# Kernel optimization log

Hardware: AMD Instinct MI355X
Metric: run time of the kernel (lower is better)

The kernel has to match this reference:

```python
import jax, jax.numpy as jnp
import numpy as np
import math

D_MODEL = 1024
NHEAD = 16
HEAD_DIM = D_MODEL // NHEAD
ROPE_BASE = 10000.0


def _rope(x):
    # x: [B, H, S, Dh]; rotate per the RoPE class (half-split variant)
    d = x.shape[-1]
    half = d // 2
    seq_len = x.shape[2]
    theta = 1.0 / (ROPE_BASE ** (jnp.arange(0, d, 2, dtype=jnp.float32) / d))  # [d/2]
    ang = jnp.arange(seq_len, dtype=jnp.float32)[:, None] * theta[None, :]      # [S, d/2]
    ang2 = jnp.concatenate([ang, ang], axis=-1)                                 # [S, d]
    cos_ = jnp.cos(ang2)[None, None, :, :]
    sin_ = jnp.sin(ang2)[None, None, :, :]
    neg_half = jnp.concatenate([-x[..., half:], x[..., :half]], axis=-1)
    return x * cos_ + neg_half * sin_


def setup_inputs() -> dict:
    key = jax.random.key(0)
    ks = jax.random.split(key, 10)
    B, S, D = 4, 2048, D_MODEL
    scale = 1.0 / math.sqrt(D)
    x = jax.random.normal(ks[0], (B, S, D), dtype=jnp.float32)
    Wq = jax.random.normal(ks[1], (D, D), dtype=jnp.float32) * scale
    bq = jnp.zeros((D,), dtype=jnp.float32)
    Wk = jax.random.normal(ks[2], (D, D), dtype=jnp.float32) * scale
    bk = jnp.zeros((D,), dtype=jnp.float32)
    Wv = jax.random.normal(ks[3], (D, D), dtype=jnp.float32) * scale
    bv = jnp.zeros((D,), dtype=jnp.float32)
    Wo = jax.random.normal(ks[4], (D, D), dtype=jnp.float32) * scale
    bo = jnp.zeros((D,), dtype=jnp.float32)
    # causal mask: mask==1 means masked (upper triangle)
    mask = jnp.triu(jnp.ones((S, S), dtype=jnp.int32), k=1)[None, None, :, :]
    return {"x": x, "Wq": Wq, "bq": bq, "Wk": Wk, "bk": bk,
            "Wv": Wv, "bv": bv, "Wo": Wo, "bo": bo, "mask": mask}


def reference(x, Wq, bq, Wk, bk, Wv, bv, Wo, bo, mask):
    B, S, D = x.shape
    H, Dh = NHEAD, HEAD_DIM

    def proj(W, b):
        y = jnp.einsum('bsd,ed->bse', x, W) + b  # torch Linear: x @ W.T + b
        return y.reshape(B, S, H, Dh).transpose(0, 2, 1, 3)  # [B,H,S,Dh]

    q = _rope(proj(Wq, bq))
    k = _rope(proj(Wk, bk))
    v = proj(Wv, bv)

    a = jnp.einsum('bhqd,bhkd->bhqk', q, k) / math.sqrt(Dh)  # [B,H,S,S]
    a = jnp.where(mask == 1, jnp.float32(-1e9), a)
    a = jax.nn.softmax(a, axis=-1)
    out = jnp.einsum('bhqk,bhkd->bhqd', a, v)                 # [B,H,S,Dh]
    out = out.transpose(0, 2, 1, 3).reshape(B, S, D)
    return jnp.einsum('bsd,ed->bse', out, Wo) + bo
```

## Files before the change

### kernel.cpp

```cpp
#include <hip/hip_runtime.h>
#include <stdint.h>

typedef unsigned short u16;
typedef __bf16 bf16x8 __attribute__((ext_vector_type(8)));
typedef __bf16 bf16x2 __attribute__((ext_vector_type(2)));
typedef float f32x4 __attribute__((ext_vector_type(4)));

#define SEQ    2048
#define NHEAD  16
#define DH     64
#define DMODEL 1024
#define NBH    64

__device__ __forceinline__ u16 cvt1(float f){
  union { __bf16 h; u16 u; } c; c.h = (__bf16)f; return c.u;
}
__device__ __forceinline__ uint32_t cvt2(float a, float b){
  union { bf16x2 v; uint32_t u; } c; c.v = bf16x2{(__bf16)a, (__bf16)b}; return c.u;
}
__device__ __forceinline__ int swz(int row){ return (((row&7)^((row>>3)&7))<<4); }

typedef const __attribute__((address_space(1))) uint32_t* gas_t;
typedef __attribute__((address_space(3))) uint32_t* las_t;
__device__ __forceinline__ void async16(const void* g, void* l){
  __builtin_amdgcn_global_load_lds((gas_t)g, (las_t)l, 16, 0, 0);
}

__global__ void prep(const float* __restrict__ x,  const float* __restrict__ Wq,
                     const float* __restrict__ Wk, const float* __restrict__ Wv,
                     const float* __restrict__ Wo,
                     u16* __restrict__ xb, u16* __restrict__ wqkv,
                     u16* __restrict__ wob, float* __restrict__ tab)
{
  const int bid = blockIdx.x, tid = threadIdx.x;
  if (bid < 6144){
    const float* src; u16* dst; int lb;
    if      (bid < 4096){ src = x;  dst = xb;              lb = bid; }
    else if (bid < 4608){ src = Wq; dst = wqkv;            lb = bid-4096; }
    else if (bid < 5120){ src = Wk; dst = wqkv + 1048576;  lb = bid-4608; }
    else if (bid < 5632){ src = Wv; dst = wqkv + 2097152;  lb = bid-5120; }
    else                { src = Wo; dst = wob;             lb = bid-5632; }
    const size_t off = (size_t)lb*2048 + tid*8;
    float4 a = *(const float4*)(src+off);
    float4 b = *(const float4*)(src+off+4);
    bf16x8 o = { (__bf16)a.x,(__bf16)a.y,(__bf16)a.z,(__bf16)a.w,
                 (__bf16)b.x,(__bf16)b.y,(__bf16)b.z,(__bf16)b.w };
    *(bf16x8*)(dst+off) = o;
  } else {
    const int t = (bid-6144)*256 + tid;
    const int s = t >> 5, j = t & 31;
    double freq = exp(-(double)(2*j)/64.0*log(10000.0));
    double ang = (double)s*freq;
    tab[s*64 + 2*j]     = (float)cos(ang);
    tab[s*64 + 2*j + 1] = (float)sin(ang);
  }
}

template<int MODE>
__global__ __launch_bounds__(256, 2)
void gemm_bt(const u16* __restrict__ A, const u16* __restrict__ W,
             const float* __restrict__ b0, const float* __restrict__ b1,
             const float* __restrict__ b2, float* __restrict__ fout,
             u16* __restrict__ dq, u16* __restrict__ dk, u16* __restrict__ dv,
             const float* __restrict__ tab)
{
  __shared__ u16 Ab[128*32];
  __shared__ u16 Bb[128*32];
  const int tid = threadIdx.x;
  const int lane = tid & 63;
  const int w = tid >> 6, wr = w >> 1, wc = w & 1;
  const int m0 = blockIdx.y * 128;
  const int n0 = blockIdx.x * 128;
  const int c0 = lane & 15, g = lane >> 4;

  f32x4 acc[4][4] = {};

  const int sr = tid >> 2;
  const int sc = (tid & 3) * 8;
  const u16* ga = A + (size_t)(m0 + sr) * DMODEL + sc;
  const u16* gb = W + (size_t)(n0 + sr) * DMODEL + sc;
  u16* la = Ab + sr*32 + sc;
  u16* lb = Bb + sr*32 + sc;

  for (int k0 = 0; k0 < DMODEL; k0 += 32) {
    __syncthreads();
    async16(ga + k0,             la);
    async16(ga + k0 + 64*DMODEL, la + 64*32);
    async16(gb + k0,             lb);
    async16(gb + k0 + 64*DMODEL, lb + 64*32);
    __syncthreads();
    bf16x8 afr[4], bfr[4];
#pragma unroll
    for (int i=0;i<4;i++) afr[i] = *(const bf16x8*)(Ab + (wr*64 + i*16 + c0)*32 + g*8);
#pragma unroll
    for (int j=0;j<4;j++) bfr[j] = *(const bf16x8*)(Bb + (wc*64 + j*16 + c0)*32 + g*8);
    __builtin_amdgcn_s_setprio(1);
#pragma unroll
    for (int i=0;i<4;i++)
#pragma unroll
      for (int j=0;j<4;j++)
        acc[i][j] = __builtin_amdgcn_mfma_f32_16x16x32_bf16(afr[i], bfr[j], acc[i][j], 0,0,0);
    __builtin_amdgcn_s_setprio(0);
  }

  const int nbase = n0 + wc*64;
  const int t = n0 >> 10;
  const float* bias = (MODE==1) ? b0 : (t==0) ? b0 : (t==1) ? b1 : b2;
  float bv4[4];
#pragma unroll
  for (int j=0;j<4;j++) bv4[j] = bias[(nbase & 1023) + j*16 + c0];

  if (MODE == 0) {
    u16* dst = (t==0) ? dq : (t==1) ? dk : dv;
    const float qs = (t==0) ? 0.18033688011f : 1.0f;
    const int h = (nbase >> 6) & (NHEAD-1);
#pragma unroll
    for (int i=0;i<4;i++){
      const int mbase = m0 + wr*64 + i*16 + g*4;
#pragma unroll
      for (int r=0;r<4;r++){
        const int mm = mbase + r;
        const int bb = mm >> 11, s = mm & (SEQ-1);
        const size_t rowbase = (((size_t)(bb*NHEAD + h))*SEQ + s)*DH;
        if (t < 2) {
#pragma unroll
          for (int j2=0;j2<2;j2++){
            const int dh = j2*16 + c0;
            const float xl = acc[i][j2][r]   + bv4[j2];
            const float xh = acc[i][j2+2][r] + bv4[j2+2];
            const float2 cs = *(const float2*)(tab + (size_t)s*64 + dh*2);
            dst[rowbase + dh]      = cvt1((xl*cs.x - xh*cs.y)*qs);
            dst[rowbase + dh + 32] = cvt1((xh*cs.x + xl*cs.y)*qs);
          }
        } else {
#pragma unroll
          for (int j=0;j<4;j++)
            dst[rowbase + j*16 + c0] = cvt1(acc[i][j][r] + bv4[j]);
        }
      }
    }
  } else {
#pragma unroll
    for (int i=0;i<4;i++){
      const int mbase = m0 + wr*64 + i*16 + g*4;
#pragma unroll
      for (int j=0;j<4;j++){
#pragma unroll
        for (int r=0;r<4;r++)
          fout[(size_t)(mbase + r) * DMODEL + nbase + j*16 + c0] = acc[i][j][r] + bv4[j];
      }
    }
  }
}

__global__ __launch_bounds__(256, 4)
void attn_fwd(const u16* __restrict__ Q, const u16* __restrict__ K,
              const u16* __restrict__ V, u16* __restrict__ O)
{
  __shared__ u16 Kb[2][64*64];
  __shared__ u16 Vt[2][64*64];
  const int bh = blockIdx.x;
  const int pair = blockIdx.y;
  const int tid = threadIdx.x, lane = tid & 63, w = tid >> 6;
  const int c0 = lane & 15, g = lane >> 4;
  const size_t hb = (size_t)bh * SEQ * DH;
  const int b = bh >> 4, h = bh & 15;

  const int boff  = tid*16;
  const int sw1   = boff  ^ swz(boff  >> 7);
  const int boff2 = boff + 4096;
  const int sw2   = boff2 ^ swz(boff2 >> 7);
  const int rp = tid >> 3, dc = tid & 7;
  const int kv0 = 2*rp;
  const int vpos = (kv0 & 0x23) | ((kv0 & 0x10) >> 2) | ((kv0 & 0x0C) << 1);
  union U4 { ushort4 v; u16 e[4]; };

#pragma unroll 1
  for (int half = 0; half < 2; half++){
    const int qt = half ? (31 - pair) : pair;
    const int qrow_base = qt*64 + w*16;
    const int jt_end = qt;
    const int q = qrow_base + c0;

    bf16x8 qf[2];
#pragma unroll
    for (int kc=0;kc<2;kc++)
      qf[kc] = *(const bf16x8*)(Q + hb + (size_t)q*DH + kc*32 + g*8);

    f32x4 oacc[4] = {};
    float mrun = -3.0e38f, lrun = 0.f;

    {
      const char* gk = (const char*)(K + hb);
      async16(gk + sw1, (char*)Kb[0] + boff);
      async16(gk + sw2, (char*)Kb[0] + boff2);
      const u16* gv = V + hb;
      U4 v0a, v0b, v1a, v1b;
      v0a.v = *(const ushort4*)(gv + (kv0  )*DH + dc*8);
      v0b.v = *(const ushort4*)(gv + (kv0  )*DH + dc*8 + 4);
      v1a.v = *(const ushort4*)(gv + (kv0+1)*DH + dc*8);
      v1b.v = *(const ushort4*)(gv + (kv0+1)*DH + dc*8 + 4);
#pragma unroll
      for (int e=0;e<8;e++){
        const int row = dc*8 + e;
        const int gbyte = row*128 + vpos*2;
        const u16 a   = (e<4) ? v0a.e[e] : v0b.e[e-4];
        const u16 bb2 = (e<4) ? v1a.e[e] : v1b.e[e-4];
        *(uint32_t*)((char*)Vt[0] + (gbyte ^ swz(row))) = (uint32_t)a | ((uint32_t)bb2 << 16);
      }
    }
    __syncthreads();

    U4 v0a, v0b, v1a, v1b;
    for (int jt = 0; jt <= jt_end; jt++){
      const int cur = jt & 1, nxt = cur ^ 1;
      const bool pre = (jt < jt_end);
      if (pre){
        const char* gk = (const char*)(K + hb + (size_t)(jt+1)*64*DH);
        async16(gk + sw1, (char*)Kb[nxt] + boff);
        async16(gk + sw2, (char*)Kb[nxt] + boff2);
        const u16* gv = V + hb + (size_t)(jt+1)*64*DH;
        v0a.v = *(const ushort4*)(gv + (kv0  )*DH + dc*8);
        v0b.v = *(const ushort4*)(gv + (kv0  )*DH + dc*8 + 4);
        v1a.v = *(const ushort4*)(gv + (kv0+1)*DH + dc*8);
        v1b.v = *(const ushort4*)(gv + (kv0+1)*DH + dc*8 + 4);
      }

      f32x4 sT[4] = {};
#pragma unroll
      for (int kc=0;kc<2;kc++){
        bf16x8 kf[4];
#pragma unroll
        for (int j=0;j<4;j++){
          const int rr = j*16 + c0;
          const int gb2 = rr*128 + kc*64 + g*16;
          kf[j] = *(const bf16x8*)((const char*)Kb[cur] + (gb2 ^ swz(rr)));
        }
        __builtin_amdgcn_s_setprio(1);
#pragma unroll
        for (int j=0;j<4;j++)
          sT[j] = __builtin_amdgcn_mfma_f32_16x16x32_bf16(kf[j], qf[kc], sT[j], 0,0,0);
        __builtin_amdgcn_s_setprio(0);
      }
      if (jt == jt_end){
#pragma unroll
        for (int j=0;j<4;j++)
#pragma unroll
          for (int r=0;r<4;r++){
            const int kv = jt*64 + j*16 + g*4 + r;
            sT[j][r] = (kv <= q) ? sT[j][r] : -3.0e38f;
          }
      }
      float mx = -3.0e38f;
#pragma unroll
      for (int j=0;j<4;j++)
#pragma unroll
        for (int r=0;r<4;r++) mx = fmaxf(mx, sT[j][r]);
      mx = fmaxf(mx, __shfl_xor(mx, 16));
      mx = fmaxf(mx, __shfl_xor(mx, 32));
      const bool grow = __any(mx > mrun + 8.0f);
      float corr = 1.0f;
      if (grow){
        const float mnew = fmaxf(mrun, mx);
        corr = exp2f(mrun - mnew);
        mrun = mnew;
      }
      bf16x8 pa0, pa1;
      float lsum = 0.f;
#pragma unroll
      for (int j=0;j<4;j++){
#pragma unroll
        for (int r=0;r<4;r++){
          const float p = exp2f(sT[j][r] - mrun);
          lsum += p;
          if (j<2) pa0[(j&1)*4 + r] = (__bf16)p;
          else     pa1[(j&1)*4 + r] = (__bf16)p;
        }
      }
      lsum += __shfl_xor(lsum, 16);
      lsum += __shfl_xor(lsum, 32);
      lrun = lrun*corr + lsum;
      if (grow){
#pragma unroll
        for (int d=0;d<4;d++)
#pragma unroll
          for (int r=0;r<4;r++) oacc[d][r] *= corr;
      }
#pragma unroll
      for (int kc=0;kc<2;kc++){
        const bf16x8 pa = kc ? pa1 : pa0;
        bf16x8 vf[4];
#pragma unroll
        for (int d=0; d<4; d++){
          const int rr = d*16 + c0;
          const int gb2 = rr*128 + kc*64 + g*16;
          vf[d] = *(const bf16x8*)((const char*)Vt[cur] + (gb2 ^ swz(rr)));
        }
        __builtin_amdgcn_s_setprio(1);
#pragma unroll
        for (int d=0; d<4; d++)
          oacc[d] = __builtin_amdgcn_mfma_f32_16x16x32_bf16(vf[d], pa, oacc[d], 0,0,0);
        __builtin_amdgcn_s_setprio(0);
      }

      if (pre){
#pragma unroll
        for (int e=0;e<8;e++){
          const int row = dc*8 + e;
          const int gbyte = row*128 + vpos*2;
          const u16 a   = (e<4) ? v0a.e[e] : v0b.e[e-4];
          const u16 bb2 = (e<4) ? v1a.e[e] : v1b.e[e-4];
          *(uint32_t*)((char*)Vt[nxt] + (gbyte ^ swz(row))) = (uint32_t)a | ((uint32_t)bb2 << 16);
        }
      }
      __syncthreads();
    }

    {
      const float inv = 1.0f / lrun;
      u16* orow = O + ((size_t)b*SEQ + q)*DMODEL + h*DH;
#pragma unroll
      for (int d=0;d<4;d++)
#pragma unroll
        for (int r2=0;r2<2;r2++)
          *(uint32_t*)(orow + d*16 + g*4 + 2*r2) =
            cvt2(oacc[d][2*r2]*inv, oacc[d][2*r2+1]*inv);
    }
  }
}

extern "C" void kernel_launch(void* const* d_in, const int* in_sizes, int n_in,
                              void* d_out, int out_size, void* d_ws, size_t ws_size,
                              hipStream_t stream)
{
  const float* x  = (const float*)d_in[0];
  const float* Wq = (const float*)d_in[1];
  const float* bq = (const float*)d_in[2];
  const float* Wk = (const float*)d_in[3];
  const float* bk = (const float*)d_in[4];
  const float* Wv = (const float*)d_in[5];
  const float* bv = (const float*)d_in[6];
  const float* Wo = (const float*)d_in[7];
  const float* bo = (const float*)d_in[8];

  const size_t MB = 1024*1024;
  char* ws = (char*)d_ws;
  u16*  xb   = (u16*)(ws);
  u16*  aw   = (u16*)(ws);
  u16*  vw   = (u16*)(ws + 16*MB);
  u16*  wqkv = (u16*)(ws + 32*MB);
  u16*  wob  = (u16*)(ws + 38*MB);
  float* tab = (float*)(ws + 41*MB);
  u16*  qw = (u16*)d_out;
  u16*  kw = (u16*)d_out + 8*MB;

  prep<<<dim3(6400), dim3(256), 0, stream>>>(x, Wq, Wk, Wv, Wo, xb, wqkv, wob, tab);

  gemm_bt<0><<<dim3(24, 64), dim3(256), 0, stream>>>(xb, wqkv, bq, bk, bv,
                                                     nullptr, qw, kw, vw, tab);

  attn_fwd<<<dim3(64, 16), dim3(256), 0, stream>>>(qw, kw, vw, aw);

  gemm_bt<1><<<dim3(8, 64), dim3(256), 0, stream>>>(aw, wob, bo, nullptr, nullptr,
                                                    (float*)d_out, nullptr, nullptr, nullptr, nullptr);
}
```

Measured before the change: 200.9 us.

## Use 256-row query tiles with 8 waves and 32x32 MFMA in attention

The attention kernel now processes 256-query tiles per block with 512 threads (8 waves of 32 rows each) instead of 64-query tiles with 4 waves. It uses 32x32x16 bf16 MFMAs, so each K/V tile staged in shared memory is reused by more queries and global K/V traffic drops. Waves whose rows are fully masked for a KV tile skip its compute but still join the barriers. The trade-offs are fewer blocks (256 instead of 1024), launch bounds allowing only one block per CU, coarser causal load balance, and idle waves on diagonal tiles.

Result: no change. 197.6 us (-1.7%).

```diff
diff --git a/kernel.cpp b/kernel.cpp
--- a/kernel.cpp
+++ b/kernel.cpp
@@ -5,6 +5,7 @@
 typedef __bf16 bf16x8 __attribute__((ext_vector_type(8)));
 typedef __bf16 bf16x2 __attribute__((ext_vector_type(2)));
 typedef float f32x4 __attribute__((ext_vector_type(4)));
+typedef float f32x16 __attribute__((ext_vector_type(16)));
 
 #define SEQ    2048
 #define NHEAD  16
@@ -153,7 +154,7 @@
   }
 }
 
-__global__ __launch_bounds__(256, 4)
+__global__ __launch_bounds__(512, 1)
 void attn_fwd(const u16* __restrict__ Q, const u16* __restrict__ K,
               const u16* __restrict__ V, u16* __restrict__ O)
 {
@@ -162,155 +163,136 @@
   const int bh = blockIdx.x;
   const int pair = blockIdx.y;
   const int tid = threadIdx.x, lane = tid & 63, w = tid >> 6;
-  const int c0 = lane & 15, g = lane >> 4;
+  const int c31 = lane & 31, hi = lane >> 5;
   const size_t hb = (size_t)bh * SEQ * DH;
   const int b = bh >> 4, h = bh & 15;
 
-  const int boff  = tid*16;
-  const int sw1   = boff  ^ swz(boff  >> 7);
-  const int boff2 = boff + 4096;
-  const int sw2   = boff2 ^ swz(boff2 >> 7);
-  const int rp = tid >> 3, dc = tid & 7;
+  const int boff = tid*16;
+  const int ksw  = boff ^ swz(boff >> 7);
+  const int rp = tid >> 4, dc = tid & 15;
   const int kv0 = 2*rp;
-  const int vpos = (kv0 & 0x23) | ((kv0 & 0x10) >> 2) | ((kv0 & 0x0C) << 1);
+  const int vpos = (kv0 & 0x33) | ((kv0 & 4) << 1) | ((kv0 & 8) >> 1);
   union U4 { ushort4 v; u16 e[4]; };
 
 #pragma unroll 1
   for (int half = 0; half < 2; half++){
-    const int qt = half ? (31 - pair) : pair;
-    const int qrow_base = qt*64 + w*16;
-    const int jt_end = qt;
-    const int q = qrow_base + c0;
-
-    bf16x8 qf[2];
-#pragma unroll
-    for (int kc=0;kc<2;kc++)
-      qf[kc] = *(const bf16x8*)(Q + hb + (size_t)q*DH + kc*32 + g*8);
-
-    f32x4 oacc[4] = {};
+    const int qt = half ? (7 - pair) : pair;
+    const int qrow_base = qt*256 + w*32;
+    const int jt_last  = 4*qt + 3;
+    const int jt_end_w = 4*qt + (w>>1);
+    const int q = qrow_base + c31;
+
+    bf16x8 qf[4];
+#pragma unroll
+    for (int kc=0;kc<4;kc++)
+      qf[kc] = *(const bf16x8*)(Q + hb + (size_t)q*DH + kc*16 + hi*8);
+
+    f32x16 oacc0 = {}, oacc1 = {};
     float mrun = -3.0e38f, lrun = 0.f;
 
     {
       const char* gk = (const char*)(K + hb);
-      async16(gk + sw1, (char*)Kb[0] + boff);
-      async16(gk + sw2, (char*)Kb[0] + boff2);
+      async16(gk + ksw, (char*)Kb[0] + boff);
       const u16* gv = V + hb;
-      U4 v0a, v0b, v1a, v1b;
-      v0a.v = *(const ushort4*)(gv + (kv0  )*DH + dc*8);
-      v0b.v = *(const ushort4*)(gv + (kv0  )*DH + dc*8 + 4);
-      v1a.v = *(const ushort4*)(gv + (kv0+1)*DH + dc*8);
-      v1b.v = *(const ushort4*)(gv + (kv0+1)*DH + dc*8 + 4);
-#pragma unroll
-      for (int e=0;e<8;e++){
-        const int row = dc*8 + e;
-        const int gbyte = row*128 + vpos*2;
-        const u16 a   = (e<4) ? v0a.e[e] : v0b.e[e-4];
-        const u16 bb2 = (e<4) ? v1a.e[e] : v1b.e[e-4];
-        *(uint32_t*)((char*)Vt[0] + (gbyte ^ swz(row))) = (uint32_t)a | ((uint32_t)bb2 << 16);
+      U4 va, vb;
+      va.v = *(const ushort4*)(gv + kv0*DH + dc*4);
+      vb.v = *(const ushort4*)(gv + (kv0+1)*DH + dc*4);
+#pragma unroll
+      for (int d=0; d<4; d++){
+        const int row = dc*4 + d;
+        *(uint32_t*)((char*)Vt[0] + ((row*128 + vpos*2) ^ swz(row))) =
+          (uint32_t)va.e[d] | ((uint32_t)vb.e[d] << 16);
       }
     }
     __syncthreads();
 
-    U4 v0a, v0b, v1a, v1b;
-    for (int jt = 0; jt <= jt_end; jt++){
+    U4 va, vb;
+    for (int jt = 0; jt <= jt_last; jt++){
       const int cur = jt & 1, nxt = cur ^ 1;
-      const bool pre = (jt < jt_end);
+      const bool pre = (jt < jt_last);
       if (pre){
         const char* gk = (const char*)(K + hb + (size_t)(jt+1)*64*DH);
-        async16(gk + sw1, (char*)Kb[nxt] + boff);
-        async16(gk + sw2, (char*)Kb[nxt] + boff2);
+        async16(gk + ksw, (char*)Kb[nxt] + boff);
         const u16* gv = V + hb + (size_t)(jt+1)*64*DH;
-        v0a.v = *(const ushort4*)(gv + (kv0  )*DH + dc*8);
-        v0b.v = *(const ushort4*)(gv + (kv0  )*DH + dc*8 + 4);
-        v1a.v = *(const ushort4*)(gv + (kv0+1)*DH + dc*8);
-        v1b.v = *(const ushort4*)(gv + (kv0+1)*DH + dc*8 + 4);
-      }
-
-      f32x4 sT[4] = {};
-#pragma unroll
-      for (int kc=0;kc<2;kc++){
-        bf16x8 kf[4];
-#pragma unroll
-        for (int j=0;j<4;j++){
-          const int rr = j*16 + c0;
-          const int gb2 = rr*128 + kc*64 + g*16;
-          kf[j] = *(const bf16x8*)((const char*)Kb[cur] + (gb2 ^ swz(rr)));
-        }
-        __builtin_amdgcn_s_setprio(1);
-#pragma unroll
-        for (int j=0;j<4;j++)
-          sT[j] = __builtin_amdgcn_mfma_f32_16x16x32_bf16(kf[j], qf[kc], sT[j], 0,0,0);
-        __builtin_amdgcn_s_setprio(0);
-      }
-      if (jt == jt_end){
-#pragma unroll
-        for (int j=0;j<4;j++)
-#pragma unroll
-          for (int r=0;r<4;r++){
-            const int kv = jt*64 + j*16 + g*4 + r;
-            sT[j][r] = (kv <= q) ? sT[j][r] : -3.0e38f;
+        va.v = *(const ushort4*)(gv + kv0*DH + dc*4);
+        vb.v = *(const ushort4*)(gv + (kv0+1)*DH + dc*4);
+      }
+
+      if (jt <= jt_end_w){
+        f32x16 sT[2] = {};
+#pragma unroll
+        for (int kc=0;kc<4;kc++){
+          const int col = (kc*16 + hi*8)*2;
+          const int r0 = c31, r1 = 32 + c31;
+          const bf16x8 kf0 = *(const bf16x8*)((const char*)Kb[cur] + ((r0*128 + col) ^ swz(r0)));
+          const bf16x8 kf1 = *(const bf16x8*)((const char*)Kb[cur] + ((r1*128 + col) ^ swz(r1)));
+          __builtin_amdgcn_s_setprio(1);
+          sT[0] = __builtin_amdgcn_mfma_f32_32x32x16_bf16(kf0, qf[kc], sT[0], 0,0,0);
+          sT[1] = __builtin_amdgcn_mfma_f32_32x32x16_bf16(kf1, qf[kc], sT[1], 0,0,0);
+          __builtin_amdgcn_s_setprio(0);
+        }
+        if (jt == jt_end_w){
+#pragma unroll
+          for (int kvb=0;kvb<2;kvb++)
+#pragma unroll
+            for (int r=0;r<16;r++){
+              const int kv = jt*64 + kvb*32 + (r&3) + 8*(r>>2) + 4*hi;
+              sT[kvb][r] = (kv <= q) ? sT[kvb][r] : -3.0e38f;
+            }
+        }
+        float mx = -3.0e38f;
+#pragma unroll
+        for (int kvb=0;kvb<2;kvb++)
+#pragma unroll
+          for (int r=0;r<16;r++) mx = fmaxf(mx, sT[kvb][r]);
+        mx = fmaxf(mx, __shfl_xor(mx, 32));
+        const bool grow = __any(mx > mrun + 8.0f);
+        float corr = 1.0f;
+        if (grow){
+          const float mnew = fmaxf(mrun, mx);
+          corr = exp2f(mrun - mnew);
+          mrun = mnew;
+        }
+        float lsum = 0.f;
+#pragma unroll
+        for (int kvb=0;kvb<2;kvb++)
+#pragma unroll
+          for (int r=0;r<16;r++){
+            const float p = exp2f(sT[kvb][r] - mrun);
+            sT[kvb][r] = p;
+            lsum += p;
           }
-      }
-      float mx = -3.0e38f;
-#pragma unroll
-      for (int j=0;j<4;j++)
-#pragma unroll
-        for (int r=0;r<4;r++) mx = fmaxf(mx, sT[j][r]);
-      mx = fmaxf(mx, __shfl_xor(mx, 16));
-      mx = fmaxf(mx, __shfl_xor(mx, 32));
-      const bool grow = __any(mx > mrun + 8.0f);
-      float corr = 1.0f;
-      if (grow){
-        const float mnew = fmaxf(mrun, mx);
-        corr = exp2f(mrun - mnew);
-        mrun = mnew;
-      }
-      bf16x8 pa0, pa1;
-      float lsum = 0.f;
-#pragma unroll
-      for (int j=0;j<4;j++){
-#pragma unroll
-        for (int r=0;r<4;r++){
-          const float p = exp2f(sT[j][r] - mrun);
-          lsum += p;
-          if (j<2) pa0[(j&1)*4 + r] = (__bf16)p;
-          else     pa1[(j&1)*4 + r] = (__bf16)p;
-        }
-      }
-      lsum += __shfl_xor(lsum, 16);
-      lsum += __shfl_xor(lsum, 32);
-      lrun = lrun*corr + lsum;
-      if (grow){
-#pragma unroll
-        for (int d=0;d<4;d++)
-#pragma unroll
-          for (int r=0;r<4;r++) oacc[d][r] *= corr;
-      }
-#pragma unroll
-      for (int kc=0;kc<2;kc++){
-        const bf16x8 pa = kc ? pa1 : pa0;
-        bf16x8 vf[4];
+        lsum += __shfl_xor(lsum, 32);
+        lrun = lrun*corr + lsum;
+        if (grow){
+#pragma unroll
+          for (int r=0;r<16;r++){ oacc0[r] *= corr; oacc1[r] *= corr; }
+        }
+#pragma unroll
+        for (int kvb=0;kvb<2;kvb++)
+#pragma unroll
+          for (int s=0;s<2;s++){
+            union { bf16x8 v; uint32_t d[4]; } pa;
+#pragma unroll
+            for (int j=0;j<4;j++)
+              pa.d[j] = cvt2(sT[kvb][s*8+2*j], sT[kvb][s*8+2*j+1]);
+            const int col = (kvb*32 + s*16 + hi*8)*2;
+            const int r0 = c31, r1 = 32 + c31;
+            const bf16x8 vf0 = *(const bf16x8*)((const char*)Vt[cur] + ((r0*128 + col) ^ swz(r0)));
+            const bf16x8 vf1 = *(const bf16x8*)((const char*)Vt[cur] + ((r1*128 + col) ^ swz(r1)));
+            __builtin_amdgcn_s_setprio(1);
+            oacc0 = __builtin_amdgcn_mfma_f32_32x32x16_bf16(vf0, pa.v, oacc0, 0,0,0);
+            oacc1 = __builtin_amdgcn_mfma_f32_32x32x16_bf16(vf1, pa.v, oacc1, 0,0,0);
+            __builtin_amdgcn_s_setprio(0);
+          }
+      }
+
+      if (pre){
 #pragma unroll
         for (int d=0; d<4; d++){
-          const int rr = d*16 + c0;
-          const int gb2 = rr*128 + kc*64 + g*16;
-          vf[d] = *(const bf16x8*)((const char*)Vt[cur] + (gb2 ^ swz(rr)));
-        }
-        __builtin_amdgcn_s_setprio(1);
-#pragma unroll
-        for (int d=0; d<4; d++)
-          oacc[d] = __builtin_amdgcn_mfma_f32_16x16x32_bf16(vf[d], pa, oacc[d], 0,0,0);
-        __builtin_amdgcn_s_setprio(0);
-      }
-
-      if (pre){
-#pragma unroll
-        for (int e=0;e<8;e++){
-          const int row = dc*8 + e;
-          const int gbyte = row*128 + vpos*2;
-          const u16 a   = (e<4) ? v0a.e[e] : v0b.e[e-4];
-          const u16 bb2 = (e<4) ? v1a.e[e] : v1b.e[e-4];
-          *(uint32_t*)((char*)Vt[nxt] + (gbyte ^ swz(row))) = (uint32_t)a | ((uint32_t)bb2 << 16);
+          const int row = dc*4 + d;
+          *(uint32_t*)((char*)Vt[nxt] + ((row*128 + vpos*2) ^ swz(row))) =
+            (uint32_t)va.e[d] | ((uint32_t)vb.e[d] << 16);
         }
       }
       __syncthreads();
@@ -320,11 +302,11 @@
       const float inv = 1.0f / lrun;
       u16* orow = O + ((size_t)b*SEQ + q)*DMODEL + h*DH;
 #pragma unroll
-      for (int d=0;d<4;d++)
-#pragma unroll
-        for (int r2=0;r2<2;r2++)
-          *(uint32_t*)(orow + d*16 + g*4 + 2*r2) =
-            cvt2(oacc[d][2*r2]*inv, oacc[d][2*r2+1]*inv);
+      for (int r2=0;r2<8;r2++){
+        const int dh0 = 2*(r2&1) + 8*(r2>>1) + 4*hi;
+        *(uint32_t*)(orow + dh0)      = cvt2(oacc0[2*r2]*inv, oacc0[2*r2+1]*inv);
+        *(uint32_t*)(orow + 32 + dh0) = cvt2(oacc1[2*r2]*inv, oacc1[2*r2+1]*inv);
+      }
     }
   }
 }
@@ -359,7 +341,7 @@
   gemm_bt<0><<<dim3(24, 64), dim3(256), 0, stream>>>(xb, wqkv, bq, bk, bv,
                                                      nullptr, qw, kw, vw, tab);
 
-  attn_fwd<<<dim3(64, 16), dim3(256), 0, stream>>>(qw, kw, vw, aw);
+  attn_fwd<<<dim3(64, 4), dim3(512), 0, stream>>>(qw, kw, vw, aw);
 
   gemm_bt<1><<<dim3(8, 64), dim3(256), 0, stream>>>(aw, wob, bo, nullptr, nullptr,
                                                     (float*)d_out, nullptr, nullptr, nullptr, nullptr);
```
